# Kernel optimization log

Hardware: AMD Instinct MI355X
Metric: run time of the kernel (lower is better)

## Reference

```python
import jax, jax.numpy as jnp
import numpy as np

V, E, B, W, S = 50000, 256, 4096, 5, 15


def setup_inputs() -> dict:
    key = jax.random.key(0)
    k0, k1, k2, k3, k4 = jax.random.split(key, 5)
    in_embed_weight = jax.random.uniform(k0, (V, E), dtype=jnp.float32, minval=-1.0, maxval=1.0)
    out_embed_weight = jax.random.uniform(k1, (V, E), dtype=jnp.float32, minval=-1.0, maxval=1.0)
    input_labels = jax.random.randint(k2, (B,), 0, V)
    out_labels = jax.random.randint(k3, (B, W), 0, V)
    noise_labels = jax.random.randint(k4, (B * W, S), 0, V)
    return {
        "in_embed_weight": in_embed_weight,
        "out_embed_weight": out_embed_weight,
        "input_labels": input_labels,
        "out_labels": out_labels,
        "noise_labels": noise_labels,
        "num_sampled": S,
    }


def reference(in_embed_weight, out_embed_weight, input_labels, out_labels, noise_labels, num_sampled):
    batch_size, window_size = out_labels.shape
    # torch: input_labels.repeat(1, W).view(-1) TILES the batch W times (not interleave)
    in_idx = jnp.tile(input_labels, window_size)              # [B*W]
    inp = in_embed_weight[in_idx]                             # [B*W, E]
    out = out_embed_weight[out_labels.reshape(-1)]            # [B*W, E]
    noise = -out_embed_weight[noise_labels]                   # [B*W, S, E] (negated)
    # log(sigmoid(<in, out>)) per positive pair
    log_target = jax.nn.log_sigmoid(jnp.sum(inp * out, axis=1))            # [B*W]
    # sum_s log(sigmoid(-<noise_s, in>)) via batched matvec
    scores = jnp.einsum('nse,ne->ns', noise, inp)                          # [B*W, S]
    sum_log_sampled = jax.nn.log_sigmoid(scores).sum(axis=1)               # [B*W]
    loss = -(log_target + sum_log_sampled).sum() / batch_size
    return loss
```

## Files before the change

### kernel.cpp

```cpp
#include <hip/hip_runtime.h>
#include <math.h>


#define EDIM 256
#define SNEG 15

__device__ __forceinline__ float dot4(float4 a, float4 b) {
    return a.x * b.x + a.y * b.y + a.z * b.z + a.w * b.w;
}

__device__ __forceinline__ float log_sigmoid_fast(float x) {
    return fminf(x, 0.0f) - __logf(1.0f + __expf(-fabsf(x)));
}

__global__ __launch_bounds__(256, 5) void neg_loss_kernel(
    const float* __restrict__ in_w,
    const float* __restrict__ out_w,
    const int* __restrict__ in_lab,
    const int* __restrict__ out_lab,
    const int* __restrict__ noise_lab,
    float* __restrict__ partials,
    int B, int BW)
{
    __shared__ float wave_sums[4];
    const int wave = threadIdx.x >> 6;
    const int lane = threadIdx.x & 63;
    const int q    = lane >> 4;
    const int t    = lane & 15;

    const int gw = blockIdx.x * 4 + wave;
    const int TW = gridDim.x * 4;

    float c = 0.0f;
    for (int j = gw; j < BW; j += TW) {
        const int jm = (B & (B - 1)) == 0 ? (j & (B - 1)) : (j % B);
        const int in_row  = in_lab[jm];
        const int out_row = out_lab[j];
        const int* nl = noise_lab + (size_t)j * SNEG;

        const float* vin_base = in_w + (size_t)in_row * EDIM + t * 4;
        float4 vi[4];
#pragma unroll
        for (int k = 0; k < 4; ++k) vi[k] = *(const float4*)(vin_base + k * 64);

#pragma unroll
        for (int r = 0; r < 4; ++r) {
            const int d = r * 4 + q;
            const int row = (d == 0) ? out_row : nl[d - 1];
            const float* rb = out_w + (size_t)row * EDIM + t * 4;
            const float4 v0 = *(const float4*)(rb + 0 * 64);
            const float4 v1 = *(const float4*)(rb + 1 * 64);
            const float4 v2 = *(const float4*)(rb + 2 * 64);
            const float4 v3 = *(const float4*)(rb + 3 * 64);

            float s = dot4(vi[0], v0) + dot4(vi[1], v1) +
                      dot4(vi[2], v2) + dot4(vi[3], v3);
            s += __shfl_xor(s, 1, 64);
            s += __shfl_xor(s, 2, 64);
            s += __shfl_xor(s, 4, 64);
            s += __shfl_xor(s, 8, 64);
            c += log_sigmoid_fast((d == 0) ? s : -s);
        }
    }

    c += __shfl_xor(c, 16, 64);
    c += __shfl_xor(c, 32, 64);

    if (lane == 0) wave_sums[wave] = c;
    __syncthreads();
    if (threadIdx.x == 0) {
        partials[blockIdx.x] =
            wave_sums[0] + wave_sums[1] + wave_sums[2] + wave_sums[3];
    }
}

__global__ __launch_bounds__(256) void reduce_kernel(
    const float* __restrict__ partials, float* __restrict__ out,
    int n, double invB)
{
    __shared__ double wsum[4];
    double t = 0.0;
    for (int i = threadIdx.x; i < n; i += 256) t += (double)partials[i];
    t += __shfl_xor(t, 32, 64);
    t += __shfl_xor(t, 16, 64);
    t += __shfl_xor(t, 8, 64);
    t += __shfl_xor(t, 4, 64);
    t += __shfl_xor(t, 2, 64);
    t += __shfl_xor(t, 1, 64);
    if ((threadIdx.x & 63) == 0) wsum[threadIdx.x >> 6] = t;
    __syncthreads();
    if (threadIdx.x == 0) {
        double s = wsum[0] + wsum[1] + wsum[2] + wsum[3];
        *out = (float)(-s * invB);
    }
}

extern "C" void kernel_launch(void* const* d_in, const int* in_sizes, int n_in,
                              void* d_out, int out_size, void* d_ws, size_t ws_size,
                              hipStream_t stream) {
    const float* in_w      = (const float*)d_in[0];
    const float* out_w     = (const float*)d_in[1];
    const int*   in_lab    = (const int*)d_in[2];
    const int*   out_lab   = (const int*)d_in[3];
    const int*   noise_lab = (const int*)d_in[4];

    const int B  = in_sizes[2];
    const int BW = in_sizes[3];

    float* partials = (float*)d_ws;
    float* out      = (float*)d_out;

    const int blocks = 1280;
    neg_loss_kernel<<<blocks, 256, 0, stream>>>(
        in_w, out_w, in_lab, out_lab, noise_lab, partials, B, BW);

    reduce_kernel<<<1, 256, 0, stream>>>(partials, out, blocks, 1.0 / (double)B);
}
```

Before: 154.2 us.

## Split embedding dimension into column slices with partial-dot buffer and combine pass

Replaces the one-wave-per-pair kernel with a slice kernel. Each block handles one of 8 column slices of 32 floats and writes 16 partial dot products per pair to a workspace buffer. A combine kernel then sums the slices, applies log-sigmoid and accumulates into a double with atomics, followed by zero and finalize kernels. The aim is to make concurrent blocks touch only a narrow column band of the embedding tables, to improve cache locality, and to reuse the input row across the W window positions. In exchange it writes and reads an extra partials buffer of about 10 MB and issues many narrow 128-byte gathers, and the old path is kept as a fallback when the workspace is too small.

```diff
diff --git a/kernel.cpp b/kernel.cpp
--- a/kernel.cpp
+++ b/kernel.cpp
@@ -4,57 +4,133 @@
 
 #define EDIM 256
 #define SNEG 15
-
-__device__ __forceinline__ float dot4(float4 a, float4 b) {
-    return a.x * b.x + a.y * b.y + a.z * b.z + a.w * b.w;
-}
+#define NSLICE 8
+#define SLICE_COLS 32
 
 __device__ __forceinline__ float log_sigmoid_fast(float x) {
     return fminf(x, 0.0f) - __logf(1.0f + __expf(-fabsf(x)));
 }
 
-__global__ __launch_bounds__(256, 5) void neg_loss_kernel(
+__global__ void zero_acc_kernel(double* acc) { *acc = 0.0; }
+
+__global__ __launch_bounds__(256, 8) void slice_dots_kernel(
     const float* __restrict__ in_w,
     const float* __restrict__ out_w,
     const int* __restrict__ in_lab,
     const int* __restrict__ out_lab,
     const int* __restrict__ noise_lab,
     float* __restrict__ partials,
+    int B, int BW, int ND)
+{
+    const int wave = threadIdx.x >> 6;
+    const int lane = threadIdx.x & 63;
+    const int g = lane >> 3;
+    const int t = lane & 7;
+    const int s = blockIdx.x & (NSLICE - 1);
+    const int stripe = blockIdx.x >> 3;
+    const int nstripe = gridDim.x >> 3;
+    const int W = BW / B;
+
+    float* pslice = partials + (size_t)s * ND;
+    const int col0 = s * SLICE_COLS + t * 4;
+
+    for (int i = stripe * 4 + wave; i < B; i += nstripe * 4) {
+        const int in_row = in_lab[i];
+        const float4 vi = *(const float4*)(in_w + (size_t)in_row * EDIM + col0);
+
+        for (int m = 0; m < W; ++m) {
+            const int j = i + m * B;
+            const int out_row = out_lab[j];
+            const int* nl = noise_lab + (size_t)j * SNEG;
+
+            const int row0 = (g == 0) ? out_row : nl[g - 1];
+            const int row1 = nl[7 + g];
+            const float4 v0 = *(const float4*)(out_w + (size_t)row0 * EDIM + col0);
+            const float4 v1 = *(const float4*)(out_w + (size_t)row1 * EDIM + col0);
+
+            float p0 = vi.x * v0.x + vi.y * v0.y + vi.z * v0.z + vi.w * v0.w;
+            float p1 = vi.x * v1.x + vi.y * v1.y + vi.z * v1.z + vi.w * v1.w;
+            p0 += __shfl_xor(p0, 1, 64);
+            p1 += __shfl_xor(p1, 1, 64);
+            p0 += __shfl_xor(p0, 2, 64);
+            p1 += __shfl_xor(p1, 2, 64);
+            p0 += __shfl_xor(p0, 4, 64);
+            p1 += __shfl_xor(p1, 4, 64);
+
+            if (t == 0) {
+                const size_t base = (size_t)j * 16;
+                pslice[base + g] = p0;
+                pslice[base + 8 + g] = p1;
+            }
+        }
+    }
+}
+
+__global__ __launch_bounds__(256) void combine_kernel(
+    const float* __restrict__ partials, double* __restrict__ acc, int ND)
+{
+    __shared__ float wsum[4];
+    const int n = blockIdx.x * 256 + threadIdx.x;
+    float c = 0.0f;
+    if (n < ND) {
+        float ssum = 0.0f;
+#pragma unroll
+        for (int s = 0; s < NSLICE; ++s) ssum += partials[(size_t)s * ND + n];
+        const float x = ((n & 15) == 0) ? ssum : -ssum;
+        c = log_sigmoid_fast(x);
+    }
+    c += __shfl_xor(c, 1, 64);
+    c += __shfl_xor(c, 2, 64);
+    c += __shfl_xor(c, 4, 64);
+    c += __shfl_xor(c, 8, 64);
+    c += __shfl_xor(c, 16, 64);
+    c += __shfl_xor(c, 32, 64);
+    if ((threadIdx.x & 63) == 0) wsum[threadIdx.x >> 6] = c;
+    __syncthreads();
+    if (threadIdx.x == 0)
+        atomicAdd(acc, (double)(wsum[0] + wsum[1] + wsum[2] + wsum[3]));
+}
+
+__global__ void finalize_kernel(const double* acc, float* out, double invB) {
+    *out = (float)(-(*acc) * invB);
+}
+
+__device__ __forceinline__ float dot4(float4 a, float4 b) {
+    return a.x * b.x + a.y * b.y + a.z * b.z + a.w * b.w;
+}
+
+__global__ __launch_bounds__(256, 5) void neg_loss_fallback(
+    const float* __restrict__ in_w, const float* __restrict__ out_w,
+    const int* __restrict__ in_lab, const int* __restrict__ out_lab,
+    const int* __restrict__ noise_lab, float* __restrict__ partials,
     int B, int BW)
 {
     __shared__ float wave_sums[4];
     const int wave = threadIdx.x >> 6;
     const int lane = threadIdx.x & 63;
-    const int q    = lane >> 4;
-    const int t    = lane & 15;
-
+    const int q = lane >> 4;
+    const int t = lane & 15;
     const int gw = blockIdx.x * 4 + wave;
     const int TW = gridDim.x * 4;
 
     float c = 0.0f;
     for (int j = gw; j < BW; j += TW) {
-        const int jm = (B & (B - 1)) == 0 ? (j & (B - 1)) : (j % B);
-        const int in_row  = in_lab[jm];
+        const int in_row = in_lab[j % B];
         const int out_row = out_lab[j];
         const int* nl = noise_lab + (size_t)j * SNEG;
-
         const float* vin_base = in_w + (size_t)in_row * EDIM + t * 4;
         float4 vi[4];
 #pragma unroll
         for (int k = 0; k < 4; ++k) vi[k] = *(const float4*)(vin_base + k * 64);
-
 #pragma unroll
         for (int r = 0; r < 4; ++r) {
             const int d = r * 4 + q;
             const int row = (d == 0) ? out_row : nl[d - 1];
             const float* rb = out_w + (size_t)row * EDIM + t * 4;
-            const float4 v0 = *(const float4*)(rb + 0 * 64);
-            const float4 v1 = *(const float4*)(rb + 1 * 64);
-            const float4 v2 = *(const float4*)(rb + 2 * 64);
-            const float4 v3 = *(const float4*)(rb + 3 * 64);
-
-            float s = dot4(vi[0], v0) + dot4(vi[1], v1) +
-                      dot4(vi[2], v2) + dot4(vi[3], v3);
+            float s = dot4(vi[0], *(const float4*)(rb + 0)) +
+                      dot4(vi[1], *(const float4*)(rb + 64)) +
+                      dot4(vi[2], *(const float4*)(rb + 128)) +
+                      dot4(vi[3], *(const float4*)(rb + 192));
             s += __shfl_xor(s, 1, 64);
             s += __shfl_xor(s, 2, 64);
             s += __shfl_xor(s, 4, 64);
@@ -62,21 +138,16 @@
             c += log_sigmoid_fast((d == 0) ? s : -s);
         }
     }
-
     c += __shfl_xor(c, 16, 64);
     c += __shfl_xor(c, 32, 64);
-
     if (lane == 0) wave_sums[wave] = c;
     __syncthreads();
-    if (threadIdx.x == 0) {
-        partials[blockIdx.x] =
-            wave_sums[0] + wave_sums[1] + wave_sums[2] + wave_sums[3];
-    }
+    if (threadIdx.x == 0)
+        partials[blockIdx.x] = wave_sums[0] + wave_sums[1] + wave_sums[2] + wave_sums[3];
 }
 
-__global__ __launch_bounds__(256) void reduce_kernel(
-    const float* __restrict__ partials, float* __restrict__ out,
-    int n, double invB)
+__global__ __launch_bounds__(256) void reduce_fallback(
+    const float* __restrict__ partials, float* __restrict__ out, int n, double invB)
 {
     __shared__ double wsum[4];
     double t = 0.0;
@@ -89,10 +160,8 @@
     t += __shfl_xor(t, 1, 64);
     if ((threadIdx.x & 63) == 0) wsum[threadIdx.x >> 6] = t;
     __syncthreads();
-    if (threadIdx.x == 0) {
-        double s = wsum[0] + wsum[1] + wsum[2] + wsum[3];
-        *out = (float)(-s * invB);
-    }
+    if (threadIdx.x == 0)
+        *out = (float)(-(wsum[0] + wsum[1] + wsum[2] + wsum[3]) * invB);
 }
 
 extern "C" void kernel_launch(void* const* d_in, const int* in_sizes, int n_in,
@@ -106,13 +175,25 @@
 
     const int B  = in_sizes[2];
     const int BW = in_sizes[3];
+    const int ND = BW * 16;
+    const size_t partial_bytes = (size_t)NSLICE * ND * sizeof(float);
 
-    float* partials = (float*)d_ws;
-    float* out      = (float*)d_out;
+    float* out = (float*)d_out;
 
-    const int blocks = 1280;
-    neg_loss_kernel<<<blocks, 256, 0, stream>>>(
-        in_w, out_w, in_lab, out_lab, noise_lab, partials, B, BW);
+    if (ws_size >= partial_bytes + 16) {
+        float* partials = (float*)d_ws;
+        double* acc = (double*)((char*)d_ws + partial_bytes);
 
-    reduce_kernel<<<1, 256, 0, stream>>>(partials, out, blocks, 1.0 / (double)B);
+        zero_acc_kernel<<<1, 1, 0, stream>>>(acc);
+        slice_dots_kernel<<<2048, 256, 0, stream>>>(
+            in_w, out_w, in_lab, out_lab, noise_lab, partials, B, BW, ND);
+        combine_kernel<<<(ND + 255) / 256, 256, 0, stream>>>(partials, acc, ND);
+        finalize_kernel<<<1, 1, 0, stream>>>(acc, out, 1.0 / (double)B);
+    } else {
+        float* partials = (float*)d_ws;
+        const int blocks = 1280;
+        neg_loss_fallback<<<blocks, 256, 0, stream>>>(
+            in_w, out_w, in_lab, out_lab, noise_lab, partials, B, BW);
+        reduce_fallback<<<1, 256, 0, stream>>>(partials, out, blocks, 1.0 / (double)B);
+    }
 }
```

Result: slower. 167.0 us (+8.3%).

## Specialize W=5 kernel: reuse input row per wave and software-pipeline row gathers

Applied to the files above, without the earlier changes.

Adds a specialized kernel for window size 5 where each wave handles one input label and loads its in-embedding row once, reusing it across all 5 window positions instead of reloading it 5 times. The 20 gather rows are prefetched as indices up front, and out-embedding rows are loaded through a 3-deep register ring buffer with scheduling barriers so memory loads overlap the dot products. The grid becomes one wave per batch element (1024 blocks) with launch bounds lowered to 4, which trades occupancy for the extra registers. A generic fallback kernel is kept for other shapes.

```diff
diff --git a/kernel.cpp b/kernel.cpp
--- a/kernel.cpp
+++ b/kernel.cpp
@@ -13,14 +13,14 @@
     return fminf(x, 0.0f) - __logf(1.0f + __expf(-fabsf(x)));
 }
 
-__global__ __launch_bounds__(256, 5) void neg_loss_kernel(
+__global__ __launch_bounds__(256, 4) void neg_loss_w5_kernel(
     const float* __restrict__ in_w,
     const float* __restrict__ out_w,
     const int* __restrict__ in_lab,
     const int* __restrict__ out_lab,
     const int* __restrict__ noise_lab,
     float* __restrict__ partials,
-    int B, int BW)
+    int B)
 {
     __shared__ float wave_sums[4];
     const int wave = threadIdx.x >> 6;
@@ -28,33 +28,104 @@
     const int q    = lane >> 4;
     const int t    = lane & 15;
 
+    const int i = blockIdx.x * 4 + wave;
+    float c = 0.0f;
+
+    if (i < B) {
+        const int in_row = in_lab[i];
+        const float* vb = in_w + (size_t)in_row * EDIM + t * 4;
+        const float4 vi0 = *(const float4*)(vb + 0);
+        const float4 vi1 = *(const float4*)(vb + 64);
+        const float4 vi2 = *(const float4*)(vb + 128);
+        const float4 vi3 = *(const float4*)(vb + 192);
+
+        int rows[20];
+#pragma unroll
+        for (int k = 0; k < 20; ++k) {
+            const int m = k >> 2;
+            const int r = k & 3;
+            const int d = r * 4 + q;
+            const int j = i + m * B;
+            rows[k] = (d == 0) ? out_lab[j]
+                               : noise_lab[(size_t)j * SNEG + (d - 1)];
+        }
+
+        float4 buf[3][4];
+#pragma unroll
+        for (int p = 0; p < 3; ++p) {
+            const float* rb = out_w + (size_t)rows[p] * EDIM + t * 4;
+            buf[p][0] = *(const float4*)(rb + 0);
+            buf[p][1] = *(const float4*)(rb + 64);
+            buf[p][2] = *(const float4*)(rb + 128);
+            buf[p][3] = *(const float4*)(rb + 192);
+        }
+        __builtin_amdgcn_sched_barrier(0);
+
+#pragma unroll
+        for (int k = 0; k < 20; ++k) {
+            const int p = k % 3;
+            float s = dot4(vi0, buf[p][0]) + dot4(vi1, buf[p][1]) +
+                      dot4(vi2, buf[p][2]) + dot4(vi3, buf[p][3]);
+            if (k + 3 < 20) {
+                const float* rb = out_w + (size_t)rows[k + 3] * EDIM + t * 4;
+                buf[p][0] = *(const float4*)(rb + 0);
+                buf[p][1] = *(const float4*)(rb + 64);
+                buf[p][2] = *(const float4*)(rb + 128);
+                buf[p][3] = *(const float4*)(rb + 192);
+            }
+            s += __shfl_xor(s, 1, 64);
+            s += __shfl_xor(s, 2, 64);
+            s += __shfl_xor(s, 4, 64);
+            s += __shfl_xor(s, 8, 64);
+            const bool pos = ((k & 3) == 0) && (q == 0);
+            c += log_sigmoid_fast(pos ? s : -s);
+            __builtin_amdgcn_sched_barrier(0);
+        }
+
+        c += __shfl_xor(c, 16, 64);
+        c += __shfl_xor(c, 32, 64);
+    }
+
+    if (lane == 0) wave_sums[wave] = c;
+    __syncthreads();
+    if (threadIdx.x == 0) {
+        partials[blockIdx.x] =
+            wave_sums[0] + wave_sums[1] + wave_sums[2] + wave_sums[3];
+    }
+}
+
+__global__ __launch_bounds__(256, 5) void neg_loss_fallback(
+    const float* __restrict__ in_w, const float* __restrict__ out_w,
+    const int* __restrict__ in_lab, const int* __restrict__ out_lab,
+    const int* __restrict__ noise_lab, float* __restrict__ partials,
+    int B, int BW)
+{
+    __shared__ float wave_sums[4];
+    const int wave = threadIdx.x >> 6;
+    const int lane = threadIdx.x & 63;
+    const int q = lane >> 4;
+    const int t = lane & 15;
     const int gw = blockIdx.x * 4 + wave;
     const int TW = gridDim.x * 4;
 
     float c = 0.0f;
     for (int j = gw; j < BW; j += TW) {
-        const int jm = (B & (B - 1)) == 0 ? (j & (B - 1)) : (j % B);
-        const int in_row  = in_lab[jm];
+        const int in_row = in_lab[j % B];
         const int out_row = out_lab[j];
         const int* nl = noise_lab + (size_t)j * SNEG;
-
         const float* vin_base = in_w + (size_t)in_row * EDIM + t * 4;
         float4 vi[4];
 #pragma unroll
         for (int k = 0; k < 4; ++k) vi[k] = *(const float4*)(vin_base + k * 64);
-
 #pragma unroll
         for (int r = 0; r < 4; ++r) {
             const int d = r * 4 + q;
             const int row = (d == 0) ? out_row : nl[d - 1];
             const float* rb = out_w + (size_t)row * EDIM + t * 4;
-            const float4 v0 = *(const float4*)(rb + 0 * 64);
-            const float4 v1 = *(const float4*)(rb + 1 * 64);
-            const float4 v2 = *(const float4*)(rb + 2 * 64);
-            const float4 v3 = *(const float4*)(rb + 3 * 64);
-
-            float s = dot4(vi[0], v0) + dot4(vi[1], v1) +
-                      dot4(vi[2], v2) + dot4(vi[3], v3);
+            float s = dot4(vi[0], *(const float4*)(rb + 0)) +
+                      dot4(vi[1], *(const float4*)(rb + 64)) +
+                      dot4(vi[2], *(const float4*)(rb + 128)) +
+                      dot4(vi[3], *(const float4*)(rb + 192));
             s += __shfl_xor(s, 1, 64);
             s += __shfl_xor(s, 2, 64);
             s += __shfl_xor(s, 4, 64);
@@ -62,16 +133,12 @@
             c += log_sigmoid_fast((d == 0) ? s : -s);
         }
     }
-
     c += __shfl_xor(c, 16, 64);
     c += __shfl_xor(c, 32, 64);
-
     if (lane == 0) wave_sums[wave] = c;
     __syncthreads();
-    if (threadIdx.x == 0) {
-        partials[blockIdx.x] =
-            wave_sums[0] + wave_sums[1] + wave_sums[2] + wave_sums[3];
-    }
+    if (threadIdx.x == 0)
+        partials[blockIdx.x] = wave_sums[0] + wave_sums[1] + wave_sums[2] + wave_sums[3];
 }
 
 __global__ __launch_bounds__(256) void reduce_kernel(
@@ -110,9 +177,17 @@
     float* partials = (float*)d_ws;
     float* out      = (float*)d_out;
 
-    const int blocks = 1280;
-    neg_loss_kernel<<<blocks, 256, 0, stream>>>(
-        in_w, out_w, in_lab, out_lab, noise_lab, partials, B, BW);
-
-    reduce_kernel<<<1, 256, 0, stream>>>(partials, out, blocks, 1.0 / (double)B);
+    if (BW == 5 * B) {
+        const int blocks = (B + 3) / 4;
+        neg_loss_w5_kernel<<<blocks, 256, 0, stream>>>(
+            in_w, out_w, in_lab, out_lab, noise_lab, partials, B);
+        reduce_kernel<<<1, 256, 0, stream>>>(partials, out, blocks,
+                                             1.0 / (double)B);
+    } else {
+        const int blocks = 1280;
+        neg_loss_fallback<<<blocks, 256, 0, stream>>>(
+            in_w, out_w, in_lab, out_lab, noise_lab, partials, B, BW);
+        reduce_kernel<<<1, 256, 0, stream>>>(partials, out, blocks,
+                                             1.0 / (double)B);
+    }
 }
```

After: 152.8 us. About the same (-0.9%).
